# Kernel optimization log

Hardware: AMD Instinct MI355X
Metric: run time of the kernel (lower is better)

The kernel has to match this reference:

```python
import jax, jax.numpy as jnp
import numpy as np

D_MODEL, D_K, D_V, H = 1024, 64, 64, 16
B, NQ, NK = 2, 2048, 2048


def setup_inputs() -> dict:
    key = jax.random.key(0)
    ks = jax.random.split(key, 12)
    hd = H * D_K
    xav = lambda k, shape: jax.random.uniform(k, shape, jnp.float32, -1.0, 1.0) * np.sqrt(6.0 / (shape[0] + shape[1]))
    return {
        "queries": jax.random.normal(ks[0], (B, NQ, D_MODEL), jnp.float32),
        "keys": jax.random.normal(ks[1], (B, NK, D_MODEL), jnp.float32),
        "values": jax.random.normal(ks[2], (B, NK, D_MODEL), jnp.float32),
        "memory": jax.random.uniform(ks[3], (B, NK), jnp.float32),
        "Wq": xav(ks[4], (D_MODEL, hd)), "bq": jnp.zeros((hd,), jnp.float32),
        "Wk": xav(ks[5], (D_MODEL, hd)), "bk": jnp.zeros((hd,), jnp.float32),
        "Wv": xav(ks[6], (D_MODEL, H * D_V)), "bv": jnp.zeros((H * D_V,), jnp.float32),
        "Wo": xav(ks[7], (H * D_V, D_MODEL)), "bo": jnp.zeros((D_MODEL,), jnp.float32),
        "Wmm": xav(ks[8], (1, H * D_V)), "bmm": jnp.zeros((H * D_V,), jnp.float32),
    }


def reference(queries, keys, values, memory, Wq, bq, Wk, bk, Wv, bv, Wo, bo, Wmm, bmm):
    b, nq = queries.shape[:2]
    nk = keys.shape[1]
    # projections -> (b, h, n, d)
    q = (queries @ Wq + bq).reshape(b, nq, H, D_K).transpose(0, 2, 1, 3)
    k = (keys @ Wk + bk).reshape(b, nk, H, D_K).transpose(0, 2, 1, 3)
    v = (values @ Wv + bv).reshape(b, nk, H, D_V).transpose(0, 2, 1, 3)
    # memory gate: fc_mm(memory[..., None]) -> (b, nk, h*d_k) -> (b, h, nk, d_k)
    mm = (memory[:, :, None] * Wmm[0] + bmm).reshape(b, nk, H, D_K).transpose(0, 2, 1, 3)
    att = jnp.einsum("bhqd,bhkd->bhqk", q, k * mm) / np.sqrt(D_K).astype(np.float32)
    att = jax.nn.softmax(att, axis=-1)
    out = jnp.einsum("bhqk,bhkd->bhqd", att, v * mm)
    out = out.transpose(0, 2, 1, 3).reshape(b, nq, H * D_V)
    return out @ Wo + bo
```

## Files before the change

### kernel.cpp

```cpp
#include <hip/hip_runtime.h>
#include <hip/hip_bf16.h>

#define H_   16
#define NQ_  2048
#define NK_  2048
#define DM_  1024

typedef float f32x4 __attribute__((ext_vector_type(4)));
typedef float f32x16 __attribute__((ext_vector_type(16)));
typedef __bf16 bf16x8 __attribute__((ext_vector_type(8)));
typedef unsigned short u16x8 __attribute__((ext_vector_type(8)));
typedef unsigned short u16x4 __attribute__((ext_vector_type(4)));

__device__ __forceinline__ unsigned short bfbits(float x) {
  __bf16 h = (__bf16)x;
  return __builtin_bit_cast(unsigned short, h);
}

__global__ __launch_bounds__(256) void prep(
    const float* __restrict__ Wq, const float* __restrict__ Wk,
    const float* __restrict__ Wv, const float* __restrict__ Wo,
    unsigned short* __restrict__ WqT, unsigned short* __restrict__ WkT,
    unsigned short* __restrict__ WvT, unsigned short* __restrict__ WoT,
    const float* __restrict__ q, const float* __restrict__ k, const float* __restrict__ v,
    unsigned short* __restrict__ qo, unsigned short* __restrict__ ko,
    unsigned short* __restrict__ vo) {
  __shared__ float t[64][65];
  const int flat = blockIdx.x;
  if (flat < 1024) {
    const int z = flat >> 8, bx = (flat >> 4) & 15, by = flat & 15;
    const float* src = (z == 0) ? Wq : (z == 1) ? Wk : (z == 2) ? Wv : Wo;
    unsigned short* dst = (z == 0) ? WqT : (z == 1) ? WkT : (z == 2) ? WvT : WoT;
    const int r0 = bx * 64, c0 = by * 64;
    for (int i = threadIdx.x; i < 4096; i += 256) {
      int r = i >> 6, c = i & 63;
      t[r][c] = src[(size_t)(r0 + r) * DM_ + c0 + c];
    }
    __syncthreads();
    for (int i = threadIdx.x; i < 4096; i += 256) {
      int n = i >> 6, kk = i & 63;
      dst[(size_t)(c0 + n) * DM_ + r0 + kk] = bfbits(t[kk][n]);
    }
  } else {
    const int tt = flat - 1024;
    const int which = tt >> 11;
    const float* src = (which == 0) ? q : (which == 1) ? k : v;
    unsigned short* dst = (which == 0) ? qo : (which == 1) ? ko : vo;
    const int i = (tt & 2047) * 256 + threadIdx.x;
    const float4* s4 = (const float4*)src;
    float4 a = s4[2 * i], b = s4[2 * i + 1];
    bf16x8 o;
    o[0] = (__bf16)a.x; o[1] = (__bf16)a.y; o[2] = (__bf16)a.z; o[3] = (__bf16)a.w;
    o[4] = (__bf16)b.x; o[5] = (__bf16)b.y; o[6] = (__bf16)b.z; o[7] = (__bf16)b.w;
    *((bf16x8*)dst + i) = o;
  }
}

__device__ __forceinline__ void gll16(const unsigned short* g, unsigned short* l) {
  __builtin_amdgcn_global_load_lds((const __attribute__((address_space(1))) void*)g,
                                   (__attribute__((address_space(3))) void*)l, 16, 0, 0);
}

template <int MODE>
__device__ __forceinline__ void gemm128_body(
    int bx, int by,
    const unsigned short* __restrict__ A, const unsigned short* __restrict__ Bt, int K,
    const float* __restrict__ bias, const float* __restrict__ mem,
    const float* __restrict__ Wmm, const float* __restrict__ bmm,
    unsigned short* __restrict__ obf,
    unsigned short* Al, unsigned short* Bl) {
  const int tid = threadIdx.x, lane = tid & 63, w = tid >> 6;
  const int wm = w >> 1, wn = w & 1;
  const int m0 = bx * 128, n0 = by * 128;
  const int lrow = lane >> 2, lcol = (lane & 3) * 8;
  const int fr = lane & 15, fk = (lane >> 4) * 8;
  constexpr int TSZ = 128 * 32;

  f32x4 acc[4][4] = {};

  const unsigned short* ag0 = A + (size_t)(m0 + w * 32 + lrow) * K + lcol;
  const unsigned short* bg0 = Bt + (size_t)(n0 + w * 32 + lrow) * K + lcol;
  const int oa0 = (w * 32) * 32, oa1 = (w * 32 + 16) * 32;
  const size_t s16K = (size_t)16 * K;

  const int KT = K >> 5;
  gll16(ag0, Al + oa0); gll16(ag0 + s16K, Al + oa1);
  gll16(bg0, Bl + oa0); gll16(bg0 + s16K, Bl + oa1);
  ag0 += 32; bg0 += 32;
  __syncthreads();

  for (int kt = 0; kt < KT; ++kt) {
    const int cb = (kt & 1) * TSZ;
    const int sb = TSZ - cb;
    if (kt + 1 < KT) {
      gll16(ag0, Al + sb + oa0); gll16(ag0 + s16K, Al + sb + oa1);
      gll16(bg0, Bl + sb + oa0); gll16(bg0 + s16K, Bl + sb + oa1);
      ag0 += 32; bg0 += 32;
    }
    bf16x8 af[4], bfr[4];
#pragma unroll
    for (int i = 0; i < 4; ++i)
      af[i] = *(const bf16x8*)&Al[cb + (wm * 64 + i * 16 + fr) * 32 + fk];
#pragma unroll
    for (int j = 0; j < 4; ++j)
      bfr[j] = *(const bf16x8*)&Bl[cb + (wn * 64 + j * 16 + fr) * 32 + fk];
#pragma unroll
    for (int i = 0; i < 4; ++i)
#pragma unroll
      for (int j = 0; j < 4; ++j)
        acc[i][j] = __builtin_amdgcn_mfma_f32_16x16x32_bf16(af[i], bfr[j], acc[i][j], 0, 0, 0);
    __syncthreads();
  }

#pragma unroll
  for (int i = 0; i < 4; ++i) {
    const int rowb = m0 + wm * 64 + i * 16 + (lane >> 4) * 4;
#pragma unroll
    for (int j = 0; j < 4; ++j) {
      const int col = n0 + wn * 64 + j * 16 + fr;
#pragma unroll
      for (int r = 0; r < 4; ++r) {
        float v = acc[i][j][r];
        int rr = rowb + r;
        if (MODE == 0) {
          int b = rr >> 11, nq = rr & 2047, h = col >> 6, d = col & 63;
          float val = (v + bias[col]) * 0.180336884f;
          obf[(((size_t)(b * H_ + h)) * NQ_ + nq) * 64 + d] = bfbits(val);
        } else if (MODE == 1) {
          int b = rr >> 11, nk = rr & 2047, h = col >> 6, d = col & 63;
          float gate = mem[b * NK_ + nk] * Wmm[col] + bmm[col];
          float val = (v + bias[col]) * gate;
          obf[(((size_t)(b * H_ + h)) * NK_ + nk) * 64 + d] = bfbits(val);
        } else {
          int b = col >> 11, key = col & 2047, h = rr >> 6, d = rr & 63;
          float gate = mem[b * NK_ + key] * Wmm[rr] + bmm[rr];
          float val = (v + bias[rr]) * gate;
          int keyp = (key & ~12) | ((key & 4) << 1) | ((key & 8) >> 1);
          obf[(((size_t)(b * H_ + h)) * 64 + d) * NK_ + keyp] = bfbits(val);
        }
      }
    }
  }
}

__global__ __launch_bounds__(256) void gemm_qkv3(
    const unsigned short* __restrict__ qbf, const unsigned short* __restrict__ kbf,
    const unsigned short* __restrict__ vbf, const unsigned short* __restrict__ WvT,
    const unsigned short* __restrict__ WqT, const unsigned short* __restrict__ WkT,
    const float* __restrict__ bq, const float* __restrict__ bk, const float* __restrict__ bv,
    const float* __restrict__ mem, const float* __restrict__ Wmm, const float* __restrict__ bmm,
    unsigned short* __restrict__ Qp, unsigned short* __restrict__ Kp,
    unsigned short* __restrict__ VpT) {
  __shared__ unsigned short Al[2 * 128 * 32];
  __shared__ unsigned short Bl[2 * 128 * 32];
  const int gid = (blockIdx.x & 7) * 96 + (blockIdx.x >> 3);
  if (gid < 256) {
    gemm128_body<0>(gid & 31, gid >> 5, qbf, WqT, 1024, bq, nullptr, nullptr, nullptr,
                    Qp, Al, Bl);
  } else if (gid < 512) {
    int bb = gid - 256;
    gemm128_body<1>(bb & 31, bb >> 5, kbf, WkT, 1024, bk, mem, Wmm, bmm, Kp, Al, Bl);
  } else {
    int bb = gid - 512;
    gemm128_body<2>(bb & 7, bb >> 3, WvT, vbf, 1024, bv, mem, Wmm, bmm, VpT, Al, Bl);
  }
}

__global__ __launch_bounds__(256) void gemm_out(
    const unsigned short* __restrict__ AO, const unsigned short* __restrict__ WoT,
    const float* __restrict__ bo, float* __restrict__ out) {
  __shared__ unsigned short Al[2 * 64 * 32];
  __shared__ unsigned short Bl[2 * 128 * 32];
  const int b = (blockIdx.x & 7) * 64 + (blockIdx.x >> 3);
  const int bx = b & 63, by = b >> 6;
  const int tid = threadIdx.x, lane = tid & 63, w = tid >> 6;
  const int wm = w >> 1, wn = w & 1;
  const int m0 = bx * 64, n0 = by * 128;
  const int lrow = lane >> 2, lcol = (lane & 3) * 8;
  const int fr = lane & 15, fk = (lane >> 4) * 8;
  const int K = 1024;
  constexpr int TA = 64 * 32, TB = 128 * 32;

  f32x4 acc[2][4] = {};

  const unsigned short* ag = AO + (size_t)(m0 + w * 16 + lrow) * K + lcol;
  const unsigned short* bg = WoT + (size_t)(n0 + w * 32 + lrow) * K + lcol;
  const int oa = (w * 16) * 32;
  const int ob0 = (w * 32) * 32, ob1 = (w * 32 + 16) * 32;
  const size_t s16K = (size_t)16 * K;

  gll16(ag, Al + oa);
  gll16(bg, Bl + ob0); gll16(bg + s16K, Bl + ob1);
  ag += 32; bg += 32;
  __syncthreads();

  for (int kt = 0; kt < 32; ++kt) {
    const int ca = (kt & 1) * TA, cbb = (kt & 1) * TB;
    const int sa = TA - ca, sbb = TB - cbb;
    if (kt + 1 < 32) {
      gll16(ag, Al + sa + oa);
      gll16(bg, Bl + sbb + ob0); gll16(bg + s16K, Bl + sbb + ob1);
      ag += 32; bg += 32;
    }
    bf16x8 af[2], bfr[4];
#pragma unroll
    for (int i = 0; i < 2; ++i)
      af[i] = *(const bf16x8*)&Al[ca + (wm * 32 + i * 16 + fr) * 32 + fk];
#pragma unroll
    for (int j = 0; j < 4; ++j)
      bfr[j] = *(const bf16x8*)&Bl[cbb + (wn * 64 + j * 16 + fr) * 32 + fk];
#pragma unroll
    for (int i = 0; i < 2; ++i)
#pragma unroll
      for (int j = 0; j < 4; ++j)
        acc[i][j] = __builtin_amdgcn_mfma_f32_16x16x32_bf16(af[i], bfr[j], acc[i][j], 0, 0, 0);
    __syncthreads();
  }

#pragma unroll
  for (int i = 0; i < 2; ++i) {
    const int rowb = m0 + wm * 32 + i * 16 + (lane >> 4) * 4;
#pragma unroll
    for (int j = 0; j < 4; ++j) {
      const int col = n0 + wn * 64 + j * 16 + fr;
#pragma unroll
      for (int r = 0; r < 4; ++r)
        out[(size_t)(rowb + r) * DM_ + col] = acc[i][j][r] + bo[col];
    }
  }
}

__global__ __launch_bounds__(256, 1) void flash_attn(const unsigned short* __restrict__ Qp,
                                                     const unsigned short* __restrict__ Kp,
                                                     const unsigned short* __restrict__ VpT,
                                                     unsigned short* __restrict__ AO) {
  __shared__ unsigned short Ks[2][128][66];
  __shared__ unsigned short Vs[2][64][130];

  const int tid = threadIdx.x, lane = tid & 63, w = tid >> 6;
  const int gid = (blockIdx.x & 7) * 32 + (blockIdx.x >> 3);
  const int bh = gid >> 3;
  const int qt = gid & 7;
  const int r31 = lane & 31, hi2 = lane >> 5;

  const unsigned short* qg = Qp + (((size_t)bh * NQ_) + qt * 256 + w * 64 + r31) * 64 + hi2 * 8;
  bf16x8 qf0[4], qf1[4];
#pragma unroll
  for (int s = 0; s < 4; ++s) {
    qf0[s] = *(const bf16x8*)&qg[s * 16];
    qf1[s] = *(const bf16x8*)&qg[32 * 64 + s * 16];
  }

  const int krow = tid >> 1, kcol = (tid & 1) * 32;
  const int vrow = tid >> 2, vcol = (tid & 3) * 32;
  const unsigned short* kg = Kp + ((size_t)bh * NK_ + krow) * 64 + kcol;
  const unsigned short* vg = VpT + ((size_t)bh * 64 + vrow) * NK_ + vcol;

  f32x16 acc00 = {}, acc10 = {}, acc01 = {}, acc11 = {};
  float l0 = 0.0f, l1 = 0.0f;

  u16x8 kr[4], vr[4];
#pragma unroll
  for (int i = 0; i < 4; ++i) {
    kr[i] = *(const u16x8*)(kg + 8 * i);
    vr[i] = *(const u16x8*)(vg + 8 * i);
  }
#pragma unroll
  for (int i = 0; i < 4; ++i) {
    *(u16x8*)&Ks[0][krow][kcol + 8 * i] = kr[i];
    *(u16x8*)&Vs[0][vrow][vcol + 8 * i] = vr[i];
  }

  for (int kt = 0; kt < 16; ++kt) {
    const int cur = kt & 1;
    __syncthreads();

    f32x16 sv0[4] = {}, sv1[4] = {};
    __builtin_amdgcn_s_setprio(1);
#pragma unroll
    for (int s = 0; s < 4; ++s) {
#pragma unroll
      for (int kb = 0; kb < 4; ++kb) {
        bf16x8 ka = *(const bf16x8*)&Ks[cur][kb * 32 + r31][s * 16 + hi2 * 8];
        sv0[kb] = __builtin_amdgcn_mfma_f32_32x32x16_bf16(ka, qf0[s], sv0[kb], 0, 0, 0);
        sv1[kb] = __builtin_amdgcn_mfma_f32_32x32x16_bf16(ka, qf1[s], sv1[kb], 0, 0, 0);
      }
    }
    __builtin_amdgcn_s_setprio(0);

    if (kt + 1 < 16) {
      const unsigned short* kn = kg + (size_t)(kt + 1) * 128 * 64;
      const unsigned short* vn = vg + (kt + 1) * 128;
#pragma unroll
      for (int i = 0; i < 4; ++i) {
        kr[i] = *(const u16x8*)(kn + 8 * i);
        vr[i] = *(const u16x8*)(vn + 8 * i);
      }
    }

    float ps0 = 0.f, ps1 = 0.f;
    bf16x8 pb0[8], pb1[8];
#pragma unroll
    for (int kb = 0; kb < 4; ++kb) {
#pragma unroll
      for (int g = 0; g < 16; ++g) {
        float pA = __builtin_amdgcn_exp2f(sv0[kb][g]);
        float pB = __builtin_amdgcn_exp2f(sv1[kb][g]);
        ps0 += pA; ps1 += pB;
        pb0[2 * kb + (g >> 3)][g & 7] = (__bf16)pA;
        pb1[2 * kb + (g >> 3)][g & 7] = (__bf16)pB;
      }
    }
    ps0 += __shfl_xor(ps0, 32); l0 += ps0;
    ps1 += __shfl_xor(ps1, 32); l1 += ps1;

    __builtin_amdgcn_s_setprio(1);
#pragma unroll
    for (int ks = 0; ks < 8; ++ks) {
      bf16x8 va0 = *(const bf16x8*)&Vs[cur][r31][ks * 16 + hi2 * 8];
      bf16x8 va1 = *(const bf16x8*)&Vs[cur][32 + r31][ks * 16 + hi2 * 8];
      acc00 = __builtin_amdgcn_mfma_f32_32x32x16_bf16(va0, pb0[ks], acc00, 0, 0, 0);
      acc10 = __builtin_amdgcn_mfma_f32_32x32x16_bf16(va1, pb0[ks], acc10, 0, 0, 0);
      acc01 = __builtin_amdgcn_mfma_f32_32x32x16_bf16(va0, pb1[ks], acc01, 0, 0, 0);
      acc11 = __builtin_amdgcn_mfma_f32_32x32x16_bf16(va1, pb1[ks], acc11, 0, 0, 0);
    }
    __builtin_amdgcn_s_setprio(0);

    if (kt + 1 < 16) {
#pragma unroll
      for (int i = 0; i < 4; ++i) {
        *(u16x8*)&Ks[cur ^ 1][krow][kcol + 8 * i] = kr[i];
        *(u16x8*)&Vs[cur ^ 1][vrow][vcol + 8 * i] = vr[i];
      }
    }
  }

  const int b = bh >> 4, h = bh & 15;
  const float linv0 = 1.0f / l0, linv1 = 1.0f / l1;
  const int qrow0 = qt * 256 + w * 64 + r31;
  const size_t rowbase0 = (((size_t)b * NQ_ + qrow0) << 10) + h * 64;
  const size_t rowbase1 = (((size_t)b * NQ_ + qrow0 + 32) << 10) + h * 64;
#pragma unroll
  for (int c = 0; c < 4; ++c) {
    u16x4 o00, o10, o01, o11;
#pragma unroll
    for (int i = 0; i < 4; ++i) {
      o00[i] = bfbits(acc00[c * 4 + i] * linv0);
      o10[i] = bfbits(acc10[c * 4 + i] * linv0);
      o01[i] = bfbits(acc01[c * 4 + i] * linv1);
      o11[i] = bfbits(acc11[c * 4 + i] * linv1);
    }
    *(u16x4*)&AO[rowbase0 + 8 * c + 4 * hi2]      = o00;
    *(u16x4*)&AO[rowbase0 + 32 + 8 * c + 4 * hi2] = o10;
    *(u16x4*)&AO[rowbase1 + 8 * c + 4 * hi2]      = o01;
    *(u16x4*)&AO[rowbase1 + 32 + 8 * c + 4 * hi2] = o11;
  }
}

extern "C" void kernel_launch(void* const* d_in, const int* in_sizes, int n_in,
                              void* d_out, int out_size, void* d_ws, size_t ws_size,
                              hipStream_t stream) {
  const float* queries = (const float*)d_in[0];
  const float* keys    = (const float*)d_in[1];
  const float* values  = (const float*)d_in[2];
  const float* memory  = (const float*)d_in[3];
  const float* Wq  = (const float*)d_in[4];
  const float* bq  = (const float*)d_in[5];
  const float* Wk  = (const float*)d_in[6];
  const float* bk  = (const float*)d_in[7];
  const float* Wv  = (const float*)d_in[8];
  const float* bv  = (const float*)d_in[9];
  const float* Wo  = (const float*)d_in[10];
  const float* bo  = (const float*)d_in[11];
  const float* Wmm = (const float*)d_in[12];
  const float* bmm = (const float*)d_in[13];

  char* ws = (char*)d_ws;
  const size_t SZ_X = (size_t)4096 * 1024 * 2;
  const size_t SZ_W = (size_t)1024 * 1024 * 2;
  unsigned short* qbf = (unsigned short*)(ws);
  unsigned short* kbf = (unsigned short*)(ws + SZ_X);
  unsigned short* vbf = (unsigned short*)(ws + 2 * SZ_X);
  unsigned short* AO  = (unsigned short*)(ws);
  size_t off = 3 * SZ_X;
  unsigned short* WqT = (unsigned short*)(ws + off); off += SZ_W;
  unsigned short* WkT = (unsigned short*)(ws + off); off += SZ_W;
  unsigned short* WvT = (unsigned short*)(ws + off); off += SZ_W;
  unsigned short* WoT = (unsigned short*)(ws + off); off += SZ_W;
  unsigned short* Qp  = (unsigned short*)(ws + off); off += SZ_X;
  unsigned short* Kp  = (unsigned short*)(ws + off); off += SZ_X;
  unsigned short* VpT = (unsigned short*)(ws + off); off += SZ_X;

  prep<<<7168, 256, 0, stream>>>(Wq, Wk, Wv, Wo, WqT, WkT, WvT, WoT,
                                 queries, keys, values, qbf, kbf, vbf);

  gemm_qkv3<<<768, 256, 0, stream>>>(qbf, kbf, vbf, WvT, WqT, WkT,
                                     bq, bk, bv, memory, Wmm, bmm, Qp, Kp, VpT);

  flash_attn<<<256, 256, 0, stream>>>(Qp, Kp, VpT, AO);

  gemm_out<<<512, 256, 0, stream>>>(AO, WoT, bo, (float*)d_out);
}
```

Baseline: 130.2 us.

## Split flash attention over key halves and merge partial outputs

Splits the key dimension of the attention kernel into two halves, doubling the grid and allowing two blocks per CU, then adds a merge kernel that sums the unnormalized bf16 partial outputs and divides by the combined row sums. This targets under-occupancy from a single wave of 256 blocks. It costs an extra launch, extra global traffic for the partials, and some precision loss from storing partials in bf16.

```diff
diff --git a/kernel.cpp b/kernel.cpp
--- a/kernel.cpp
+++ b/kernel.cpp
@@ -15,6 +15,10 @@
 __device__ __forceinline__ unsigned short bfbits(float x) {
   __bf16 h = (__bf16)x;
   return __builtin_bit_cast(unsigned short, h);
+}
+__device__ __forceinline__ float bf2f(unsigned short h) {
+  unsigned int u = ((unsigned int)h) << 16;
+  return __builtin_bit_cast(float, u);
 }
 
 __global__ __launch_bounds__(256) void prep(
@@ -230,16 +234,18 @@
   }
 }
 
-__global__ __launch_bounds__(256, 1) void flash_attn(const unsigned short* __restrict__ Qp,
+__global__ __launch_bounds__(256, 2) void flash_attn(const unsigned short* __restrict__ Qp,
                                                      const unsigned short* __restrict__ Kp,
                                                      const unsigned short* __restrict__ VpT,
-                                                     unsigned short* __restrict__ AO) {
+                                                     unsigned short* __restrict__ Opart,
+                                                     float* __restrict__ lsum) {
   __shared__ unsigned short Ks[2][128][66];
   __shared__ unsigned short Vs[2][64][130];
 
   const int tid = threadIdx.x, lane = tid & 63, w = tid >> 6;
-  const int gid = (blockIdx.x & 7) * 32 + (blockIdx.x >> 3);
-  const int bh = gid >> 3;
+  const int gid = (blockIdx.x & 7) * 64 + (blockIdx.x >> 3);
+  const int half = gid >> 8;
+  const int bh = (gid >> 3) & 31;
   const int qt = gid & 7;
   const int r31 = lane & 31, hi2 = lane >> 5;
 
@@ -253,8 +259,8 @@
 
   const int krow = tid >> 1, kcol = (tid & 1) * 32;
   const int vrow = tid >> 2, vcol = (tid & 3) * 32;
-  const unsigned short* kg = Kp + ((size_t)bh * NK_ + krow) * 64 + kcol;
-  const unsigned short* vg = VpT + ((size_t)bh * 64 + vrow) * NK_ + vcol;
+  const unsigned short* kg = Kp + ((size_t)bh * NK_ + half * 1024 + krow) * 64 + kcol;
+  const unsigned short* vg = VpT + ((size_t)bh * 64 + vrow) * NK_ + half * 1024 + vcol;
 
   f32x16 acc00 = {}, acc10 = {}, acc01 = {}, acc11 = {};
   float l0 = 0.0f, l1 = 0.0f;
@@ -271,7 +277,7 @@
     *(u16x8*)&Vs[0][vrow][vcol + 8 * i] = vr[i];
   }
 
-  for (int kt = 0; kt < 16; ++kt) {
+  for (int kt = 0; kt < 8; ++kt) {
     const int cur = kt & 1;
     __syncthreads();
 
@@ -288,7 +294,7 @@
     }
     __builtin_amdgcn_s_setprio(0);
 
-    if (kt + 1 < 16) {
+    if (kt + 1 < 8) {
       const unsigned short* kn = kg + (size_t)(kt + 1) * 128 * 64;
       const unsigned short* vn = vg + (kt + 1) * 128;
 #pragma unroll
@@ -326,7 +332,7 @@
     }
     __builtin_amdgcn_s_setprio(0);
 
-    if (kt + 1 < 16) {
+    if (kt + 1 < 8) {
 #pragma unroll
       for (int i = 0; i < 4; ++i) {
         *(u16x8*)&Ks[cur ^ 1][krow][kcol + 8 * i] = kr[i];
@@ -336,25 +342,49 @@
   }
 
   const int b = bh >> 4, h = bh & 15;
-  const float linv0 = 1.0f / l0, linv1 = 1.0f / l1;
   const int qrow0 = qt * 256 + w * 64 + r31;
-  const size_t rowbase0 = (((size_t)b * NQ_ + qrow0) << 10) + h * 64;
-  const size_t rowbase1 = (((size_t)b * NQ_ + qrow0 + 32) << 10) + h * 64;
+  unsigned short* ob0 = Opart + (((size_t)half * 4096 + b * 2048 + qrow0) << 10) + h * 64 + 4 * hi2;
+  unsigned short* ob1 = ob0 + ((size_t)32 << 10);
 #pragma unroll
   for (int c = 0; c < 4; ++c) {
     u16x4 o00, o10, o01, o11;
 #pragma unroll
     for (int i = 0; i < 4; ++i) {
-      o00[i] = bfbits(acc00[c * 4 + i] * linv0);
-      o10[i] = bfbits(acc10[c * 4 + i] * linv0);
-      o01[i] = bfbits(acc01[c * 4 + i] * linv1);
-      o11[i] = bfbits(acc11[c * 4 + i] * linv1);
-    }
-    *(u16x4*)&AO[rowbase0 + 8 * c + 4 * hi2]      = o00;
-    *(u16x4*)&AO[rowbase0 + 32 + 8 * c + 4 * hi2] = o10;
-    *(u16x4*)&AO[rowbase1 + 8 * c + 4 * hi2]      = o01;
-    *(u16x4*)&AO[rowbase1 + 32 + 8 * c + 4 * hi2] = o11;
-  }
+      o00[i] = bfbits(acc00[c * 4 + i]);
+      o10[i] = bfbits(acc10[c * 4 + i]);
+      o01[i] = bfbits(acc01[c * 4 + i]);
+      o11[i] = bfbits(acc11[c * 4 + i]);
+    }
+    *(u16x4*)(ob0 + 8 * c)      = o00;
+    *(u16x4*)(ob0 + 32 + 8 * c) = o10;
+    *(u16x4*)(ob1 + 8 * c)      = o01;
+    *(u16x4*)(ob1 + 32 + 8 * c) = o11;
+  }
+  if (hi2 == 0) {
+    lsum[((size_t)half * 32 + bh) * 2048 + qrow0]      = l0;
+    lsum[((size_t)half * 32 + bh) * 2048 + qrow0 + 32] = l1;
+  }
+}
+
+__global__ __launch_bounds__(256) void merge_halves(const unsigned short* __restrict__ Opart,
+                                                    const float* __restrict__ lsum,
+                                                    unsigned short* __restrict__ AO) {
+  const int i = blockIdx.x * 256 + threadIdx.x;
+  const int row = i >> 7;
+  const int d8 = (i & 127) * 8;
+  const int b = row >> 11, q = row & 2047, h = d8 >> 6;
+  const int bh = b * 16 + h;
+  const unsigned short* p1 = Opart + ((size_t)row << 10) + d8;
+  const unsigned short* p2 = p1 + ((size_t)4096 << 10);
+  float l1 = lsum[(size_t)bh * 2048 + q];
+  float l2 = lsum[((size_t)32 + bh) * 2048 + q];
+  float inv = 1.0f / (l1 + l2);
+  u16x8 a = *(const u16x8*)p1;
+  u16x8 c = *(const u16x8*)p2;
+  u16x8 o;
+#pragma unroll
+  for (int j = 0; j < 8; ++j) o[j] = bfbits((bf2f(a[j]) + bf2f(c[j])) * inv);
+  *(u16x8*)&AO[((size_t)row << 10) + d8] = o;
 }
 
 extern "C" void kernel_launch(void* const* d_in, const int* in_sizes, int n_in,
@@ -376,20 +406,20 @@
   const float* bmm = (const float*)d_in[13];
 
   char* ws = (char*)d_ws;
-  const size_t SZ_X = (size_t)4096 * 1024 * 2;
-  const size_t SZ_W = (size_t)1024 * 1024 * 2;
-  unsigned short* qbf = (unsigned short*)(ws);
-  unsigned short* kbf = (unsigned short*)(ws + SZ_X);
-  unsigned short* vbf = (unsigned short*)(ws + 2 * SZ_X);
-  unsigned short* AO  = (unsigned short*)(ws);
-  size_t off = 3 * SZ_X;
-  unsigned short* WqT = (unsigned short*)(ws + off); off += SZ_W;
-  unsigned short* WkT = (unsigned short*)(ws + off); off += SZ_W;
-  unsigned short* WvT = (unsigned short*)(ws + off); off += SZ_W;
-  unsigned short* WoT = (unsigned short*)(ws + off); off += SZ_W;
-  unsigned short* Qp  = (unsigned short*)(ws + off); off += SZ_X;
-  unsigned short* Kp  = (unsigned short*)(ws + off); off += SZ_X;
-  unsigned short* VpT = (unsigned short*)(ws + off); off += SZ_X;
+  const size_t MB = 1024 * 1024;
+  unsigned short* qbf   = (unsigned short*)(ws);
+  unsigned short* AO    = (unsigned short*)(ws);
+  unsigned short* kbf   = (unsigned short*)(ws + 8 * MB);
+  unsigned short* vbf   = (unsigned short*)(ws + 16 * MB);
+  unsigned short* Opart = (unsigned short*)(ws + 8 * MB);
+  float*          lsum  = (float*)(ws + 24 * MB);
+  unsigned short* WqT   = (unsigned short*)(ws + 26 * MB);
+  unsigned short* WkT   = (unsigned short*)(ws + 28 * MB);
+  unsigned short* WvT   = (unsigned short*)(ws + 30 * MB);
+  unsigned short* WoT   = (unsigned short*)(ws + 32 * MB);
+  unsigned short* Qp    = (unsigned short*)(ws + 34 * MB);
+  unsigned short* Kp    = (unsigned short*)(ws + 42 * MB);
+  unsigned short* VpT   = (unsigned short*)(ws + 50 * MB);
 
   prep<<<7168, 256, 0, stream>>>(Wq, Wk, Wv, Wo, WqT, WkT, WvT, WoT,
                                  queries, keys, values, qbf, kbf, vbf);
@@ -397,7 +427,9 @@
   gemm_qkv3<<<768, 256, 0, stream>>>(qbf, kbf, vbf, WvT, WqT, WkT,
                                      bq, bk, bv, memory, Wmm, bmm, Qp, Kp, VpT);
 
-  flash_attn<<<256, 256, 0, stream>>>(Qp, Kp, VpT, AO);
+  flash_attn<<<512, 256, 0, stream>>>(Qp, Kp, VpT, Opart, lsum);
+
+  merge_halves<<<2048, 256, 0, stream>>>(Opart, lsum, AO);
 
   gemm_out<<<512, 256, 0, stream>>>(AO, WoT, bo, (float*)d_out);
 }
```

Result: slower. 136.2 us (+4.7%).
